# Kernel tuning notes

Measured on AMD Instinct MI355X. Metric: run time of the kernel, lower is better.

Reference implementation:

```python
import jax, jax.numpy as jnp
import numpy as np

N, D, H, L, B, DFF = 100000, 256, 8, 64, 4096, 1024
HD = D // H  # head_dim
EPS = 1e-5


def _xavier(k, shape):
    lim = (6.0 / (shape[0] + shape[1])) ** 0.5
    return jax.random.uniform(k, shape, jnp.float32, -lim, lim)


def setup_inputs() -> dict:
    key = jax.random.key(0)
    ks = jax.random.split(key, 12)
    batch = jax.random.randint(ks[0], (B,), 0, N)
    nei_idx = jax.random.randint(ks[1], (B, L), 0, N)
    # faithful to neis_ = [[k] + neighbor[k] ...]: self node is first neighbor
    nei_idx = nei_idx.at[:, 0].set(batch)
    lengths = jax.random.randint(ks[2], (B,), 1, L + 1)
    nei_mask = jnp.arange(L)[None, :] >= lengths[:, None]  # True = NaN padding
    embeddings = jax.random.normal(ks[3], (N, D), jnp.float32)
    return {
        "batch": batch, "nei_idx": nei_idx, "nei_mask": nei_mask,
        "embeddings": embeddings,
        "Wq": _xavier(ks[4], (D, D)), "bq": jnp.zeros((D,), jnp.float32),
        "Wk": _xavier(ks[5], (D, D)), "bk": jnp.zeros((D,), jnp.float32),
        "Wv": _xavier(ks[6], (D, D)), "bv": jnp.zeros((D,), jnp.float32),
        "Wo": _xavier(ks[7], (D, D)), "bo": jnp.zeros((D,), jnp.float32),
        "W1": _xavier(ks[8], (D, DFF)), "b1": jnp.zeros((DFF,), jnp.float32),
        "W2": _xavier(ks[9], (DFF, D)), "b2": jnp.zeros((D,), jnp.float32),
        "ln1_w": jnp.ones((D,), jnp.float32), "ln1_b": jnp.zeros((D,), jnp.float32),
        "ln2_w": jnp.ones((D,), jnp.float32), "ln2_b": jnp.zeros((D,), jnp.float32),
    }


def _layer_norm(y, w, b):
    mu = y.mean(-1, keepdims=True)
    var = ((y - mu) ** 2).mean(-1, keepdims=True)
    return (y - mu) / jnp.sqrt(var + EPS) * w + b


def reference(batch, nei_idx, nei_mask, embeddings,
              Wq, bq, Wk, bk, Wv, bv, Wo, bo,
              W1, b1, W2, b2, ln1_w, ln1_b, ln2_w, ln2_b):
    x = embeddings[batch]        # [B, D]  query-node embeddings
    nei = embeddings[nei_idx]    # [B, L, D] gathered (padded) neighbor embeds
    q = ((x @ Wq + bq) * (HD ** -0.5)).reshape(B, H, HD)
    k = (nei @ Wk + bk).reshape(B, L, H, HD)
    v = (nei @ Wv + bv).reshape(B, L, H, HD)
    scores = jnp.einsum('bhd,blhd->bhl', q, k)          # single-query attn
    scores = jnp.where(nei_mask[:, None, :], -jnp.inf, scores)
    att = jax.nn.softmax(scores, axis=-1)               # [B, H, L]
    attout = jnp.einsum('bhl,blhd->bhd', att, v).reshape(B, D) @ Wo + bo
    s = _layer_norm(x + attout, ln1_w, ln1_b)
    # note: original applies relu after BOTH linear1 and linear2
    f = jax.nn.relu(jax.nn.relu(s @ W1 + b1) @ W2 + b2)
    return _layer_norm(s + f, ln2_w, ln2_b)
```

## Files before the change

### kernel.cpp

```cpp
#include <hip/hip_runtime.h>
#include <hip/hip_bf16.h>
#include <math.h>

#define BQ   4096
#define D    256
#define NH   8
#define HD   32
#define LN_  64
#define DFF  1024
#define EPSV 1e-5f
#define QSCALE 0.17677669529663687f

typedef __attribute__((ext_vector_type(8))) short short8;
typedef __attribute__((ext_vector_type(4))) float f32x4;

#define ESWZ(row, byte) ((byte) ^ (((row) & 7) << 4))

__device__ __forceinline__ float wave_sum(float v){
#pragma unroll
  for (int off = 32; off; off >>= 1) v += __shfl_xor(v, off, 64);
  return v;
}
__device__ __forceinline__ unsigned short f2bf(float f){
  __hip_bfloat16 h = __float2bfloat16(f);
  unsigned short r; __builtin_memcpy(&r, &h, 2); return r;
}
__device__ __forceinline__ unsigned pk2(float a, float b){
  __hip_bfloat162 h = __float22bfloat162_rn(make_float2(a, b));
  unsigned r; __builtin_memcpy(&r, &h, 4); return r;
}
__device__ __forceinline__ float bflo(unsigned u){ return __uint_as_float(u << 16); }
__device__ __forceinline__ float bfhi(unsigned u){ return __uint_as_float(u & 0xFFFF0000u); }

__global__ __launch_bounds__(256) void k_prep(
    const float* __restrict__ Wq, const float* __restrict__ Wk,
    const float* __restrict__ Wv, const float* __restrict__ Wo,
    const float* __restrict__ W1, const float* __restrict__ W2,
    const float* __restrict__ bq, const float* __restrict__ bv,
    const float* __restrict__ bo,
    const int* __restrict__ batch, const float* __restrict__ emb,
    const unsigned int* __restrict__ maskw,
    unsigned short* __restrict__ W1t, unsigned short* __restrict__ W2t,
    unsigned short* __restrict__ Mt, unsigned short* __restrict__ Gt,
    float* __restrict__ pb, float* __restrict__ bo2,
    float* __restrict__ X, unsigned short* __restrict__ Xb,
    int* __restrict__ flagsArr){
  __shared__ float smem[4224];
  const int bid = blockIdx.x;
  const int tid = threadIdx.x;

  if (bid < 128){
    const float* src; unsigned short* dst; int K, N, t0;
    if (bid < 64){ src = W1; dst = W1t; K = 256;  N = 1024; t0 = bid; }
    else         { src = W2; dst = W2t; K = 1024; N = 256;  t0 = bid - 64; }
    const int ntx = N / 64;
    const int k0 = (t0 / ntx) * 64, n0 = (t0 % ntx) * 64;
    float (*Ts)[65] = (float(*)[65])smem;
    {
      int r = tid >> 2, c4 = (tid & 3) * 16;
#pragma unroll
      for (int i = 0; i < 4; i++)
        *(float4*)&Ts[r][c4 + i * 4] = *(const float4*)(src + (size_t)(k0 + r) * N + n0 + c4 + i * 4);
    }
    __syncthreads();
    {
      int n = tid >> 2, kc = (tid & 3) * 16;
      unsigned int pk[8];
#pragma unroll
      for (int i = 0; i < 8; i++)
        pk[i] = pk2(Ts[kc + 2 * i][n], Ts[kc + 2 * i + 1][n]);
      unsigned short* orow = dst + (size_t)(n0 + n) * K + k0 + kc;
      *(uint4*)(orow)     = *(uint4*)&pk[0];
      *(uint4*)(orow + 8) = *(uint4*)&pk[4];
    }
    return;
  }
  if (bid < 256){
    int t0 = bid - 128;
    int hd0 = (t0 & 31) * 64, c0 = (t0 >> 5) * 64;
    int h = hd0 >> 8, d0 = hd0 & 255;
    float (*WqS)[33] = (float(*)[33])smem;
    float (*WkS)[33] = (float(*)[33])(smem + 64 * 33);
#pragma unroll
    for (int s = 0; s < 2; s++){
      int idx = tid + s * 256;
      int row = idx >> 3, c4 = (idx & 7) * 4;
      *(float4*)&WqS[row][c4] = *(const float4*)(Wq + (size_t)(c0 + row) * 256 + h * 32 + c4);
      *(float4*)&WkS[row][c4] = *(const float4*)(Wk + (size_t)(d0 + row) * 256 + h * 32 + c4);
    }
    __syncthreads();
    int jo = (tid >> 4) * 4, io = (tid & 15) * 4;
    float acc[4][4];
#pragma unroll
    for (int j = 0; j < 4; j++)
#pragma unroll
      for (int i = 0; i < 4; i++) acc[j][i] = 0.f;
#pragma unroll
    for (int t = 0; t < 32; t++){
#pragma unroll
      for (int j = 0; j < 4; j++){
        float kv = WkS[jo + j][t];
#pragma unroll
        for (int i = 0; i < 4; i++) acc[j][i] = fmaf(kv, WqS[io + i][t], acc[j][i]);
      }
    }
#pragma unroll
    for (int j = 0; j < 4; j++){
      uint2 o;
      o.x = pk2(acc[j][0] * QSCALE, acc[j][1] * QSCALE);
      o.y = pk2(acc[j][2] * QSCALE, acc[j][3] * QSCALE);
      *(uint2*)(Mt + (size_t)(hd0 + jo + j) * 256 + c0 + io) = o;
    }
    if (c0 == 0 && tid < 64){
      float s = 0.f;
#pragma unroll
      for (int t = 0; t < 32; t++) s = fmaf(WkS[tid][t], bq[h * 32 + t], s);
      pb[hd0 + tid] = s * QSCALE;
    }
    return;
  }
  if (bid < 384){
    int t0 = bid - 256;
    int hd0 = (t0 & 31) * 64, n0 = (t0 >> 5) * 64;
    int h = hd0 >> 8, d0 = hd0 & 255;
    float (*WvS)[33] = (float(*)[33])smem;
    float (*WoS)[65] = (float(*)[65])(smem + 64 * 33);
#pragma unroll
    for (int s = 0; s < 2; s++){
      int idx = tid + s * 256;
      int row = idx >> 3, c4 = (idx & 7) * 4;
      *(float4*)&WvS[row][c4] = *(const float4*)(Wv + (size_t)(d0 + row) * 256 + h * 32 + c4);
      int row2 = idx >> 4, c42 = (idx & 15) * 4;
      *(float4*)&WoS[row2][c42] = *(const float4*)(Wo + (size_t)(h * 32 + row2) * 256 + n0 + c42);
    }
    __syncthreads();
    int jo = (tid >> 4) * 4, io = (tid & 15) * 4;
    float acc[4][4];
#pragma unroll
    for (int i = 0; i < 4; i++)
#pragma unroll
      for (int j = 0; j < 4; j++) acc[i][j] = 0.f;
#pragma unroll
    for (int t = 0; t < 32; t++){
#pragma unroll
      for (int i = 0; i < 4; i++){
        float ov = WoS[t][io + i];
#pragma unroll
        for (int j = 0; j < 4; j++) acc[i][j] = fmaf(ov, WvS[jo + j][t], acc[i][j]);
      }
    }
#pragma unroll
    for (int i = 0; i < 4; i++){
      uint2 o;
      o.x = pk2(acc[i][0], acc[i][1]);
      o.y = pk2(acc[i][2], acc[i][3]);
      *(uint2*)(Gt + (size_t)(n0 + io + i) * 2048 + hd0 + jo) = o;
    }
    return;
  }
  if (bid == 384){
    int n = tid;
    float s = bo[n];
    for (int j = 0; j < 256; j++) s = fmaf(bv[j], Wo[(size_t)j * 256 + n], s);
    bo2[n] = s;
    return;
  }
  if (bid < 641){
    int* df = (int*)smem;
    if (tid == 0) df[0] = 0;
    __syncthreads();
    int idx = (bid - 385) * 256 + tid;
    unsigned int v = maskw[idx];
    int bits = 0;
    if (v == 0x3F800000u) bits = 2;
    else if (v & 0xFFFFFF00u) bits = 1;
    int b2 = __any(bits & 2) ? 2 : 0;
    int b1 = __any(bits & 1) ? 1 : 0;
    if ((tid & 63) == 0 && (b1 | b2)) atomicOr(df, b1 | b2);
    __syncthreads();
    if (tid == 0) flagsArr[bid - 385] = df[0];
    return;
  }
  {
    int gid = (bid - 641) * 256 + tid;
    int b = gid >> 6, c = gid & 63;
    float4 v = ((const float4*)(emb + (size_t)batch[b] * D))[c];
    ((float4*)(X + (size_t)b * D))[c] = v;
    uint2 p;
    p.x = pk2(v.x, v.y);
    p.y = pk2(v.z, v.w);
    ((uint2*)Xb)[gid] = p;
  }
}

template<int BM, int BN, int EPI, bool OUTBF>
__global__ __launch_bounds__(256) void k_mgemm(const unsigned short* __restrict__ A,
                                               const unsigned short* __restrict__ Bt,
                                               const float* __restrict__ bias,
                                               void* __restrict__ Cout,
                                               int M, int N, int K){
  constexpr int BK = 64;
  constexpr int WM = BM / 2, WN = BN / 2;
  constexpr int MR = WM / 16, NR = WN / 16;
  constexpr int AIT = BM * 8 / 256;
  constexpr int BIT = BN * 8 / 256;
  __shared__ __align__(16) unsigned short As[BM * BK];
  __shared__ __align__(16) unsigned short Bs[BN * BK];
  char* ab = (char*)As; char* bb = (char*)Bs;
  const int tid = threadIdx.x;
  const int w = tid >> 6, lane = tid & 63;
  const int wm = w >> 1, wn = w & 1;
  const int gx = gridDim.x;
  const int nwg = gx * gridDim.y;
  const int o = blockIdx.y * gx + blockIdx.x;
  const int lin = (o & 7) * (nwg >> 3) + (o >> 3);
  const int row0 = (lin / gx) * BM, col0 = (lin % gx) * BN;
  f32x4 acc[MR][NR];
#pragma unroll
  for (int m = 0; m < MR; m++)
#pragma unroll
    for (int n = 0; n < NR; n++) acc[m][n] = (f32x4){0.f, 0.f, 0.f, 0.f};

  for (int k0 = 0; k0 < K; k0 += BK){
#pragma unroll
    for (int s = 0; s < AIT; s++){
      int c = s * 256 + tid;
      int r = c >> 3, jj = c & 7;
      uint4 v = *(const uint4*)(A + (size_t)(row0 + r) * K + k0 + jj * 8);
      *(uint4*)(ab + ESWZ(r, r * 128 + jj * 16)) = v;
    }
#pragma unroll
    for (int s = 0; s < BIT; s++){
      int c = s * 256 + tid;
      int r = c >> 3, jj = c & 7;
      uint4 v = *(const uint4*)(Bt + (size_t)(col0 + r) * K + k0 + jj * 8);
      *(uint4*)(bb + ESWZ(r, r * 128 + jj * 16)) = v;
    }
    __syncthreads();
#pragma unroll
    for (int kk = 0; kk < 2; kk++){
      short8 af[MR], bf[NR];
#pragma unroll
      for (int m = 0; m < MR; m++){
        int r = wm * WM + m * 16 + (lane & 15);
        af[m] = *(const short8*)(ab + ESWZ(r, r * 128 + (kk * 4 + (lane >> 4)) * 16));
      }
#pragma unroll
      for (int n = 0; n < NR; n++){
        int r = wn * WN + n * 16 + (lane & 15);
        bf[n] = *(const short8*)(bb + ESWZ(r, r * 128 + (kk * 4 + (lane >> 4)) * 16));
      }
#pragma unroll
      for (int m = 0; m < MR; m++)
#pragma unroll
        for (int n = 0; n < NR; n++)
          acc[m][n] = __builtin_amdgcn_mfma_f32_16x16x32_bf16(af[m], bf[n], acc[m][n], 0, 0, 0);
    }
    __syncthreads();
  }
#pragma unroll
  for (int m = 0; m < MR; m++){
#pragma unroll
    for (int n = 0; n < NR; n++){
      int col = col0 + wn * WN + n * 16 + (lane & 15);
      float bsv = bias[col];
      int rbase = row0 + wm * WM + m * 16 + (lane >> 4) * 4;
#pragma unroll
      for (int r = 0; r < 4; r++){
        float v = acc[m][n][r] + bsv;
        if (EPI == 3) v = fmaxf(v, 0.f);
        if (OUTBF) ((unsigned short*)Cout)[(size_t)(rbase + r) * N + col] = f2bf(v);
        else       ((float*)Cout)[(size_t)(rbase + r) * N + col] = v;
      }
    }
  }
}

__global__ __launch_bounds__(256) void k_attn(const int* __restrict__ nei_idx,
                                              const void* __restrict__ nei_mask,
                                              const int* __restrict__ flagsArr,
                                              const float* __restrict__ emb,
                                              const unsigned short* __restrict__ Pb,
                                              unsigned short* __restrict__ Cb){
  const int b = blockIdx.x;
  const int tid = threadIdx.x;
  const int w = tid >> 6, lane = tid & 63;
  __shared__ __align__(16) unsigned short EbfH[64 * 128];
  __shared__ __align__(16) unsigned short Pl[9 * 256];
  __shared__ float sc[NH * LN_];
  __shared__ float mskv[LN_];
  __shared__ int   fred[4];
  char* eb = (char*)EbfH;
  char* pl = (char*)Pl;
  unsigned* pfu = (unsigned*)EbfH;

  {
    int f = flagsArr[tid];
#pragma unroll
    for (int off = 32; off; off >>= 1) f |= __shfl_xor(f, off, 64);
    if (lane == 0) fred[w] = f;
  }
  float4 vr[16];
#pragma unroll
  for (int i = 0; i < 16; i++){
    int nid = nei_idx[(size_t)b * LN_ + w * 16 + i];
    vr[i] = ((const float4*)(emb + (size_t)nid * D))[lane];
  }
  {
    int r = tid >> 5, cb16 = (tid & 31) * 16;
    uint4 v = *(const uint4*)((const char*)Pb + (size_t)b * 4096 + r * 512 + cb16);
    *(uint4*)(pl + ESWZ(r, r * 512 + cb16)) = v;
  }
  if (tid < 64) *(uint2*)(pl + 8 * 512 + tid * 8) = make_uint2(0u, 0u);
  __syncthreads();

  if (tid < LN_){
    int fl = fred[0] | fred[1] | fred[2] | fred[3];
    int mf = (fl & 2) ? 2 : ((fl & 1) ? 1 : 0);
    bool m;
    if (mf == 1)      m = ((const unsigned char*)nei_mask)[(size_t)b * LN_ + tid] != 0;
    else if (mf == 2) m = ((const float*)nei_mask)[(size_t)b * LN_ + tid] != 0.f;
    else              m = ((const int*)nei_mask)[(size_t)b * LN_ + tid] != 0;
    mskv[tid] = m ? 1.f : 0.f;
  }

  f32x4 acc = {0.f, 0.f, 0.f, 0.f};
  const int hr = lane & 15;
  const int arow = hr < 8 ? hr : 8;
  const int bl = w * 16 + (lane & 15);
  const int koff = (lane >> 4) * 16;
#pragma unroll
  for (int half = 0; half < 2; half++){
    if ((lane >> 5) == half){
      int cl = lane & 31;
#pragma unroll
      for (int i = 0; i < 16; i++){
        int l = w * 16 + i;
        uint2 p;
        p.x = pk2(vr[i].x, vr[i].y);
        p.y = pk2(vr[i].z, vr[i].w);
        *(uint2*)(eb + ESWZ(l, l * 256 + cl * 8)) = p;
      }
    }
    __syncthreads();
    __builtin_amdgcn_s_setprio(1);
#pragma unroll
    for (int kk = 0; kk < 4; kk++){
      int kabs = half * 4 + kk;
      short8 af = *(const short8*)(pl + ESWZ(arow, arow * 512 + kabs * 64 + koff));
      short8 bf = *(const short8*)(eb + ESWZ(bl, bl * 256 + kk * 64 + koff));
      acc = __builtin_amdgcn_mfma_f32_16x16x32_bf16(af, bf, acc, 0, 0, 0);
    }
    __builtin_amdgcn_s_setprio(0);
    __syncthreads();
  }
  {
    int hb = (lane >> 4) * 4;
    if (hb < 8){
#pragma unroll
      for (int r = 0; r < 4; r++) sc[(hb + r) * LN_ + bl] = acc[r];
    }
  }
  __syncthreads();

  {
    int h = tid >> 5, j = tid & 31;
    float v0 = mskv[j]      > 0.5f ? -INFINITY : sc[h * LN_ + j];
    float v1 = mskv[j + 32] > 0.5f ? -INFINITY : sc[h * LN_ + j + 32];
    float m = fmaxf(v0, v1);
#pragma unroll
    for (int off = 16; off; off >>= 1) m = fmaxf(m, __shfl_xor(m, off, 64));
    float e0 = __expf(v0 - m), e1 = __expf(v1 - m);
    float s = e0 + e1;
#pragma unroll
    for (int off = 16; off; off >>= 1) s += __shfl_xor(s, off, 64);
    float inv = 1.f / s;
    sc[h * LN_ + j]      = e0 * inv;
    sc[h * LN_ + j + 32] = e1 * inv;
  }
  __syncthreads();

  {
    float4 pacc[NH];
#pragma unroll
    for (int h = 0; h < NH; h++) pacc[h] = make_float4(0.f, 0.f, 0.f, 0.f);
#pragma unroll
    for (int i = 0; i < 16; i++){
      int l = w * 16 + i;
#pragma unroll
      for (int h = 0; h < NH; h++){
        float t = sc[h * LN_ + l];
        pacc[h].x = fmaf(t, vr[i].x, pacc[h].x);
        pacc[h].y = fmaf(t, vr[i].y, pacc[h].y);
        pacc[h].z = fmaf(t, vr[i].z, pacc[h].z);
        pacc[h].w = fmaf(t, vr[i].w, pacc[h].w);
      }
    }
#pragma unroll
    for (int h = 0; h < NH; h++){
      uint2 p;
      p.x = pk2(pacc[h].x, pacc[h].y);
      p.y = pk2(pacc[h].z, pacc[h].w);
      *(uint2*)&pfu[w * 1024 + h * 128 + lane * 2] = p;
    }
  }
  __syncthreads();

#pragma unroll
  for (int s = 0; s < 2; s++){
    int gi = tid + s * 256;
    int h = gi >> 6, d4 = gi & 63;
    float x = 0.f, y = 0.f, z = 0.f, u = 0.f;
#pragma unroll
    for (int wv = 0; wv < 4; wv++){
      uint2 p = *(uint2*)&pfu[wv * 1024 + h * 128 + d4 * 2];
      x += bflo(p.x); y += bfhi(p.x);
      z += bflo(p.y); u += bfhi(p.y);
    }
    uint2 o;
    o.x = pk2(x, y);
    o.y = pk2(z, u);
    *(uint2*)(Cb + (size_t)b * 2048 + h * 256 + d4 * 4) = o;
  }
}

__global__ __launch_bounds__(256) void k_ln(const float* __restrict__ A,
                                            const float* __restrict__ Bv,
                                            const float* __restrict__ w,
                                            const float* __restrict__ bi,
                                            float* __restrict__ out,
                                            unsigned short* __restrict__ outb){
  const int row = blockIdx.x, tid = threadIdx.x;
  const int wv = tid >> 6, lane = tid & 63;
  __shared__ float red[8];
  float v = A[(size_t)row * D + tid] + Bv[(size_t)row * D + tid];
  float s = wave_sum(v);
  if (lane == 0) red[wv] = s;
  __syncthreads();
  float mu = (red[0] + red[1] + red[2] + red[3]) * (1.f / D);
  float d = v - mu;
  float s2 = wave_sum(d * d);
  if (lane == 0) red[4 + wv] = s2;
  __syncthreads();
  float var = (red[4] + red[5] + red[6] + red[7]) * (1.f / D);
  float res = d * rsqrtf(var + EPSV) * w[tid] + bi[tid];
  out[(size_t)row * D + tid] = res;
  if (outb) outb[(size_t)row * D + tid] = f2bf(res);
}

extern "C" void kernel_launch(void* const* d_in, const int* in_sizes, int n_in,
                              void* d_out, int out_size, void* d_ws, size_t ws_size,
                              hipStream_t stream){
  (void)in_sizes; (void)n_in; (void)out_size; (void)ws_size;
  const int*   batch    = (const int*)d_in[0];
  const int*   nei_idx  = (const int*)d_in[1];
  const void*  nei_mask = d_in[2];
  const float* emb      = (const float*)d_in[3];
  const float* Wq = (const float*)d_in[4];  const float* bq = (const float*)d_in[5];
  const float* Wk = (const float*)d_in[6];
  const float* Wv = (const float*)d_in[8];  const float* bv = (const float*)d_in[9];
  const float* Wo = (const float*)d_in[10]; const float* bo = (const float*)d_in[11];
  const float* W1 = (const float*)d_in[12]; const float* b1 = (const float*)d_in[13];
  const float* W2 = (const float*)d_in[14]; const float* b2 = (const float*)d_in[15];
  const float* ln1w = (const float*)d_in[16]; const float* ln1b = (const float*)d_in[17];
  const float* ln2w = (const float*)d_in[18]; const float* ln2b = (const float*)d_in[19];

  float* ws = (float*)d_ws;
  float* X  = ws;
  float* Y  = ws + (size_t)1 * 1048576;
  float* S  = ws + (size_t)2 * 1048576;
  float* F  = ws + (size_t)3 * 1048576;
  unsigned short* Pbf = (unsigned short*)(ws + (size_t)4 * 1048576);
  unsigned short* Cb  = Pbf;
  unsigned short* Sb  = (unsigned short*)(ws + (size_t)8 * 1048576);
  unsigned short* HHb = (unsigned short*)(ws + (size_t)9 * 1048576);
  unsigned short* Xb  = (unsigned short*)(ws + (size_t)11 * 1048576);
  char* wb = (char*)(ws + (size_t)12 * 1048576);
  unsigned short* W1t = (unsigned short*)(wb);
  unsigned short* W2t = (unsigned short*)(wb + (512u << 10));
  unsigned short* Mt  = (unsigned short*)(wb + (1024u << 10));
  unsigned short* Gt  = (unsigned short*)(wb + (2048u << 10));
  float* pbv  = (float*)(wb + (3072u << 10));
  float* bo2  = (float*)(wb + (3072u << 10) + 8192);
  int*   flagsArr = (int*)(wb + (3072u << 10) + 16384);
  float* out = (float*)d_out;

  k_prep<<<1665, 256, 0, stream>>>(Wq, Wk, Wv, Wo, W1, W2, bq, bv, bo,
                                   batch, emb, (const unsigned int*)nei_mask,
                                   W1t, W2t, Mt, Gt, pbv, bo2, X, Xb, flagsArr);
  k_mgemm<128, 64, 2, true><<<dim3(2048 / 64, BQ / 128), 256, 0, stream>>>(Xb, Mt, pbv, Pbf, BQ, 2048, 256);
  k_attn<<<BQ, 256, 0, stream>>>(nei_idx, nei_mask, flagsArr, emb, Pbf, Cb);
  k_mgemm<32, 64, 2, false><<<dim3(D / 64, BQ / 32), 256, 0, stream>>>(Cb, Gt, bo2, Y, BQ, D, 2048);
  k_ln<<<BQ, 256, 0, stream>>>(X, Y, ln1w, ln1b, S, Sb);
  k_mgemm<128, 64, 3, true><<<dim3(DFF / 64, BQ / 128), 256, 0, stream>>>(Sb, W1t, b1, HHb, BQ, DFF, 256);
  k_mgemm<32, 64, 3, false><<<dim3(D / 64, BQ / 32), 256, 0, stream>>>(HHb, W2t, b2, F, BQ, D, DFF);
  k_ln<<<BQ, 256, 0, stream>>>(S, F, ln2w, ln2b, out, nullptr);
}
```

Before: 119.6 us.

## Fuse embedding gather into projection GEMM and fuse LayerNorm into output GEMMs

```diff
diff --git a/kernel.cpp b/kernel.cpp
--- a/kernel.cpp
+++ b/kernel.cpp
@@ -38,12 +38,10 @@
     const float* __restrict__ W1, const float* __restrict__ W2,
     const float* __restrict__ bq, const float* __restrict__ bv,
     const float* __restrict__ bo,
-    const int* __restrict__ batch, const float* __restrict__ emb,
     const unsigned int* __restrict__ maskw,
     unsigned short* __restrict__ W1t, unsigned short* __restrict__ W2t,
     unsigned short* __restrict__ Mt, unsigned short* __restrict__ Gt,
     float* __restrict__ pb, float* __restrict__ bo2,
-    float* __restrict__ X, unsigned short* __restrict__ Xb,
     int* __restrict__ flagsArr){
   __shared__ float smem[4224];
   const int bid = blockIdx.x;
@@ -165,7 +163,7 @@
     bo2[n] = s;
     return;
   }
-  if (bid < 641){
+  {
     int* df = (int*)smem;
     if (tid == 0) df[0] = 0;
     __syncthreads();
@@ -179,17 +177,86 @@
     if ((tid & 63) == 0 && (b1 | b2)) atomicOr(df, b1 | b2);
     __syncthreads();
     if (tid == 0) flagsArr[bid - 385] = df[0];
-    return;
-  }
-  {
-    int gid = (bid - 641) * 256 + tid;
-    int b = gid >> 6, c = gid & 63;
-    float4 v = ((const float4*)(emb + (size_t)batch[b] * D))[c];
-    ((float4*)(X + (size_t)b * D))[c] = v;
-    uint2 p;
-    p.x = pk2(v.x, v.y);
-    p.y = pk2(v.z, v.w);
-    ((uint2*)Xb)[gid] = p;
+  }
+}
+
+__global__ __launch_bounds__(256) void k_pg(const int* __restrict__ batch,
+                                            const float* __restrict__ emb,
+                                            const unsigned short* __restrict__ Bt,
+                                            const float* __restrict__ bias,
+                                            unsigned short* __restrict__ Cout){
+  constexpr int BM = 128, BN = 64, BK = 64, K = 256, N = 2048;
+  constexpr int WM = 64, WN = 32, MR = 4, NR = 2;
+  __shared__ __align__(16) unsigned short As[BM * BK];
+  __shared__ __align__(16) unsigned short Bs[BN * BK];
+  char* ab = (char*)As; char* bb = (char*)Bs;
+  const int tid = threadIdx.x;
+  const int w = tid >> 6, lane = tid & 63;
+  const int wm = w >> 1, wn = w & 1;
+  const int gx = gridDim.x;
+  const int nwg = gx * gridDim.y;
+  const int o = blockIdx.y * gx + blockIdx.x;
+  const int lin = (o & 7) * (nwg >> 3) + (o >> 3);
+  const int row0 = (lin / gx) * BM, col0 = (lin % gx) * BN;
+  f32x4 acc[MR][NR];
+#pragma unroll
+  for (int m = 0; m < MR; m++)
+#pragma unroll
+    for (int n = 0; n < NR; n++) acc[m][n] = (f32x4){0.f, 0.f, 0.f, 0.f};
+
+  for (int k0 = 0; k0 < K; k0 += BK){
+#pragma unroll
+    for (int s = 0; s < 4; s++){
+      int c = s * 256 + tid;
+      int r = c >> 3, jj = c & 7;
+      const float* src = emb + (size_t)batch[row0 + r] * D + k0 + jj * 8;
+      float4 v0 = *(const float4*)(src);
+      float4 v1 = *(const float4*)(src + 4);
+      uint4 pk;
+      pk.x = pk2(v0.x, v0.y); pk.y = pk2(v0.z, v0.w);
+      pk.z = pk2(v1.x, v1.y); pk.w = pk2(v1.z, v1.w);
+      *(uint4*)(ab + ESWZ(r, r * 128 + jj * 16)) = pk;
+    }
+#pragma unroll
+    for (int s = 0; s < 2; s++){
+      int c = s * 256 + tid;
+      int r = c >> 3, jj = c & 7;
+      uint4 v = *(const uint4*)(Bt + (size_t)(col0 + r) * K + k0 + jj * 8);
+      *(uint4*)(bb + ESWZ(r, r * 128 + jj * 16)) = v;
+    }
+    __syncthreads();
+#pragma unroll
+    for (int kk = 0; kk < 2; kk++){
+      short8 af[MR], bf[NR];
+#pragma unroll
+      for (int m = 0; m < MR; m++){
+        int r = wm * WM + m * 16 + (lane & 15);
+        af[m] = *(const short8*)(ab + ESWZ(r, r * 128 + (kk * 4 + (lane >> 4)) * 16));
+      }
+#pragma unroll
+      for (int n = 0; n < NR; n++){
+        int r = wn * WN + n * 16 + (lane & 15);
+        bf[n] = *(const short8*)(bb + ESWZ(r, r * 128 + (kk * 4 + (lane >> 4)) * 16));
+      }
+#pragma unroll
+      for (int m = 0; m < MR; m++)
+#pragma unroll
+        for (int n = 0; n < NR; n++)
+          acc[m][n] = __builtin_amdgcn_mfma_f32_16x16x32_bf16(af[m], bf[n], acc[m][n], 0, 0, 0);
+    }
+    __syncthreads();
+  }
+#pragma unroll
+  for (int m = 0; m < MR; m++){
+#pragma unroll
+    for (int n = 0; n < NR; n++){
+      int col = col0 + wn * WN + n * 16 + (lane & 15);
+      float bsv = bias[col];
+      int rbase = row0 + wm * WM + m * 16 + (lane >> 4) * 4;
+#pragma unroll
+      for (int r = 0; r < 4; r++)
+        Cout[(size_t)(rbase + r) * N + col] = f2bf(acc[m][n][r] + bsv);
+    }
   }
 }
 
@@ -276,6 +343,100 @@
   }
 }
 
+template<bool RELU, bool GX, bool WBF>
+__global__ __launch_bounds__(256) void k_gln(const unsigned short* __restrict__ A,
+                                             const unsigned short* __restrict__ Bt,
+                                             const float* __restrict__ bias,
+                                             const int* __restrict__ batch,
+                                             const float* __restrict__ emb,
+                                             const float* __restrict__ residP,
+                                             const float* __restrict__ lnw,
+                                             const float* __restrict__ lnb,
+                                             float* __restrict__ outF,
+                                             unsigned short* __restrict__ outB,
+                                             int K){
+  constexpr int NR = 4;
+  __shared__ __align__(16) unsigned short As[16 * 64];
+  __shared__ __align__(16) unsigned short Bs[256 * 64];
+  char* ab = (char*)As; char* bb = (char*)Bs;
+  const int tid = threadIdx.x;
+  const int w = tid >> 6, lane = tid & 63;
+  const int row0 = blockIdx.x * 16;
+  f32x4 acc[NR];
+#pragma unroll
+  for (int n = 0; n < NR; n++) acc[n] = (f32x4){0.f, 0.f, 0.f, 0.f};
+
+  for (int k0 = 0; k0 < K; k0 += 64){
+    if (tid < 128){
+      int r = tid >> 3, jj = tid & 7;
+      uint4 v = *(const uint4*)(A + (size_t)(row0 + r) * K + k0 + jj * 8);
+      *(uint4*)(ab + ESWZ(r, r * 128 + jj * 16)) = v;
+    }
+#pragma unroll
+    for (int s = 0; s < 8; s++){
+      int c = s * 256 + tid;
+      int r = c >> 3, jj = c & 7;
+      uint4 v = *(const uint4*)(Bt + (size_t)r * K + k0 + jj * 8);
+      *(uint4*)(bb + ESWZ(r, r * 128 + jj * 16)) = v;
+    }
+    __syncthreads();
+#pragma unroll
+    for (int kk = 0; kk < 2; kk++){
+      int r = lane & 15;
+      short8 af = *(const short8*)(ab + ESWZ(r, r * 128 + (kk * 4 + (lane >> 4)) * 16));
+#pragma unroll
+      for (int n = 0; n < NR; n++){
+        int rb = w * 64 + n * 16 + (lane & 15);
+        short8 bf = *(const short8*)(bb + ESWZ(rb, rb * 128 + (kk * 4 + (lane >> 4)) * 16));
+        acc[n] = __builtin_amdgcn_mfma_f32_16x16x32_bf16(af, bf, acc[n], 0, 0, 0);
+      }
+    }
+    __syncthreads();
+  }
+  float* sf = (float*)Bs;
+#pragma unroll
+  for (int n = 0; n < NR; n++){
+    int col = w * 64 + n * 16 + (lane & 15);
+    float bsv = bias[col];
+#pragma unroll
+    for (int r = 0; r < 4; r++){
+      int row = (lane >> 4) * 4 + r;
+      float v = acc[n][r] + bsv;
+      if (RELU) v = fmaxf(v, 0.f);
+      float rv;
+      if (GX) rv = emb[(size_t)batch[row0 + row] * D + col];
+      else    rv = residP[(size_t)(row0 + row) * D + col];
+      sf[row * 257 + col] = v + rv;
+    }
+  }
+  __syncthreads();
+  {
+    int row = tid >> 4, seg = tid & 15;
+    float vals[16];
+    float s = 0.f, s2 = 0.f;
+#pragma unroll
+    for (int j = 0; j < 16; j++){
+      float v = sf[row * 257 + seg * 16 + j];
+      vals[j] = v; s += v; s2 += v * v;
+    }
+#pragma unroll
+    for (int off = 8; off; off >>= 1){
+      s += __shfl_xor(s, off, 64);
+      s2 += __shfl_xor(s2, off, 64);
+    }
+    float mu = s * (1.f / 256.f);
+    float var = s2 * (1.f / 256.f) - mu * mu;
+    float rstd = rsqrtf(var + EPSV);
+#pragma unroll
+    for (int j = 0; j < 16; j++){
+      int col = seg * 16 + j;
+      float res = (vals[j] - mu) * rstd * lnw[col] + lnb[col];
+      outF[(size_t)(row0 + row) * D + col] = res;
+      if (WBF) outB[(size_t)(row0 + row) * D + col] = f2bf(res);
+    }
+  }
+}
+
 __global__ __launch_bounds__(256) void k_attn(const int* __restrict__ nei_idx,
                                               const void* __restrict__ nei_mask,
                                               const int* __restrict__ flagsArr,
@@ -424,30 +585,6 @@
   }
 }
 
-__global__ __launch_bounds__(256) void k_ln(const float* __restrict__ A,
-                                            const float* __restrict__ Bv,
-                                            const float* __restrict__ w,
-                                            const float* __restrict__ bi,
-                                            float* __restrict__ out,
-                                            unsigned short* __restrict__ outb){
-  const int row = blockIdx.x, tid = threadIdx.x;
-  const int wv = tid >> 6, lane = tid & 63;
-  __shared__ float red[8];
-  float v = A[(size_t)row * D + tid] + Bv[(size_t)row * D + tid];
-  float s = wave_sum(v);
-  if (lane == 0) red[wv] = s;
-  __syncthreads();
-  float mu = (red[0] + red[1] + red[2] + red[3]) * (1.f / D);
-  float d = v - mu;
-  float s2 = wave_sum(d * d);
-  if (lane == 0) red[4 + wv] = s2;
-  __syncthreads();
-  float var = (red[4] + red[5] + red[6] + red[7]) * (1.f / D);
-  float res = d * rsqrtf(var + EPSV) * w[tid] + bi[tid];
-  out[(size_t)row * D + tid] = res;
-  if (outb) outb[(size_t)row * D + tid] = f2bf(res);
-}
-
 extern "C" void kernel_launch(void* const* d_in, const int* in_sizes, int n_in,
                               void* d_out, int out_size, void* d_ws, size_t ws_size,
                               hipStream_t stream){
@@ -466,15 +603,11 @@
   const float* ln2w = (const float*)d_in[18]; const float* ln2b = (const float*)d_in[19];
 
   float* ws = (float*)d_ws;
-  float* X  = ws;
-  float* Y  = ws + (size_t)1 * 1048576;
   float* S  = ws + (size_t)2 * 1048576;
-  float* F  = ws + (size_t)3 * 1048576;
   unsigned short* Pbf = (unsigned short*)(ws + (size_t)4 * 1048576);
   unsigned short* Cb  = Pbf;
   unsigned short* Sb  = (unsigned short*)(ws + (size_t)8 * 1048576);
   unsigned short* HHb = (unsigned short*)(ws + (size_t)9 * 1048576);
-  unsigned short* Xb  = (unsigned short*)(ws + (size_t)11 * 1048576);
   char* wb = (char*)(ws + (size_t)12 * 1048576);
   unsigned short* W1t = (unsigned short*)(wb);
   unsigned short* W2t = (unsigned short*)(wb + (512u << 10));
@@ -485,14 +618,14 @@
   int*   flagsArr = (int*)(wb + (3072u << 10) + 16384);
   float* out = (float*)d_out;
 
-  k_prep<<<1665, 256, 0, stream>>>(Wq, Wk, Wv, Wo, W1, W2, bq, bv, bo,
-                                   batch, emb, (const unsigned int*)nei_mask,
-                                   W1t, W2t, Mt, Gt, pbv, bo2, X, Xb, flagsArr);
-  k_mgemm<128, 64, 2, true><<<dim3(2048 / 64, BQ / 128), 256, 0, stream>>>(Xb, Mt, pbv, Pbf, BQ, 2048, 256);
+  k_prep<<<641, 256, 0, stream>>>(Wq, Wk, Wv, Wo, W1, W2, bq, bv, bo,
+                                  (const unsigned int*)nei_mask,
+                                  W1t, W2t, Mt, Gt, pbv, bo2, flagsArr);
+  k_pg<<<dim3(2048 / 64, BQ / 128), 256, 0, stream>>>(batch, emb, Mt, pbv, Pbf);
   k_attn<<<BQ, 256, 0, stream>>>(nei_idx, nei_mask, flagsArr, emb, Pbf, Cb);
-  k_mgemm<32, 64, 2, false><<<dim3(D / 64, BQ / 32), 256, 0, stream>>>(Cb, Gt, bo2, Y, BQ, D, 2048);
-  k_ln<<<BQ, 256, 0, stream>>>(X, Y, ln1w, ln1b, S, Sb);
+  k_gln<false, true, true><<<BQ / 16, 256, 0, stream>>>(Cb, Gt, bo2, batch, emb, nullptr,
+                                                        ln1w, ln1b, S, Sb, 2048);
   k_mgemm<128, 64, 3, true><<<dim3(DFF / 64, BQ / 128), 256, 0, stream>>>(Sb, W1t, b1, HHb, BQ, DFF, 256);
-  k_mgemm<32, 64, 3, false><<<dim3(D / 64, BQ / 32), 256, 0, stream>>>(HHb, W2t, b2, F, BQ, D, DFF);
-  k_ln<<<BQ, 256, 0, stream>>>(S, F, ln2w, ln2b, out, nullptr);
-}
+  k_gln<true, false, false><<<BQ / 16, 256, 0, stream>>>(HHb, W2t, b2, nullptr, nullptr, S,
+                                                         ln2w, ln2b, out, nullptr, 1024);
+}
```

Result: slower. 137.1 us (+14.6%).
